# Kernel optimization log

Hardware: AMD Instinct MI355X
Metric: run time of the kernel (lower is better)

## Reference

```python
import jax, jax.numpy as jnp
import numpy as np

# Dims
B, L = 64, 64            # bs*n_vars, patch_num
C, K = 32, 100           # cluster_num, top-k tokens per cluster
D_MODEL, H, D_LLM = 128, 8, 768
D_KEYS = D_MODEL // H    # 16
TEMP = 1.0 / np.sqrt(D_KEYS)
SCALE = 0.02             # param init scale for numerical stability


def setup_inputs() -> dict:
    key = jax.random.key(0)
    ks = jax.random.split(key, 8)
    return {
        "topk_token_embeddings": jax.random.normal(ks[0], (C, K, D_LLM), jnp.float32),
        "ts_emb": jax.random.normal(ks[1], (B, L, D_MODEL), jnp.float32),
        "cluster_probs": jax.random.uniform(ks[2], (B, L, C), jnp.float32),
        # per-cluster projections; last input column is a fused bias (+1 dim)
        "Wq": jax.random.normal(ks[3], (C, H * D_KEYS, D_MODEL + 1), jnp.float32) * SCALE,
        "Wk": jax.random.normal(ks[4], (C, H * D_KEYS, D_LLM + 1), jnp.float32) * SCALE,
        "Wv": jax.random.normal(ks[5], (C, H * D_KEYS, D_LLM + 1), jnp.float32) * SCALE,
        "Wo": jax.random.normal(ks[6], (C, H, D_KEYS, D_LLM), jnp.float32) * SCALE,
        "bo": jax.random.normal(ks[7], (C, D_LLM), jnp.float32) * SCALE,
    }


def reference(topk_token_embeddings, ts_emb, cluster_probs, Wq, Wk, Wv, Wo, bo):
    # Per-cluster Q projection: (B,L,C,H*dk) -> (B,L,C,H,dk)
    q = jnp.einsum('bld,cgd->blcg', ts_emb, Wq[..., :-1]) + Wq[..., -1]
    q = q.reshape(B, L, C, H, D_KEYS)
    # Per-cluster K/V projections: (K,C,H*dk) -> (K,C,H,dk)
    k = jnp.einsum('ckd,cgd->kcg', topk_token_embeddings, Wk[..., :-1]) + Wk[..., -1]
    k = k.reshape(K, C, H, D_KEYS)
    v = jnp.einsum('ckd,cgd->kcg', topk_token_embeddings, Wv[..., :-1]) + Wv[..., -1]
    v = v.reshape(K, C, H, D_KEYS)
    # Attention over token axis k with extra cluster axis c
    att = jnp.einsum('blchd,kchd->bchlk', q, k)          # (B,C,H,L,K)
    att = jax.nn.softmax(TEMP * att, axis=-1)            # dropout is identity in eval
    out = jnp.einsum('bchlk,kchd->bclhd', att, v)        # (B,C,L,H,dk)
    # Per-cluster output projection to d_llm
    aligned = jnp.einsum('bclhd,chde->blce', out, Wo) + bo  # (B,L,C,d_llm)
    # TSAligner: cluster-probability weighted sum over clusters
    fused = jnp.sum(aligned * cluster_probs[:, :, :, None], axis=-2)  # (B,L,d_llm)
    return fused
```

## Files before the change

### kernel.cpp

```cpp
#include <hip/hip_runtime.h>
#include <stdint.h>

#define NB 64
#define NL 64
#define NC 32
#define NK 100
#define NH 8
#define DKEY 16
#define DM 128
#define NG 128
#define DLLM 768
#define KP 4128
#define TEMP 0.25f

typedef __attribute__((ext_vector_type(8))) short bf16x8;
typedef __attribute__((ext_vector_type(4))) short bf16x4;
typedef __attribute__((ext_vector_type(4))) float f32x4;

typedef uint32_t __attribute__((address_space(1))) gu32;
typedef uint32_t __attribute__((address_space(3))) lu32;

__device__ __forceinline__ void gload_lds16(const void* g, void* l) {
    __builtin_amdgcn_global_load_lds((const gu32*)g, (lu32*)l, 16, 0, 0);
}

__device__ __forceinline__ uint16_t f2bf(float f) {
    union { float f; uint32_t i; } x; x.f = f;
    uint32_t r = x.i + 0x7FFFu + ((x.i >> 16) & 1u);
    return (uint16_t)(r >> 16);
}
__device__ __forceinline__ uint32_t pack2(float lo, float hi) {
    return (uint32_t)f2bf(lo) | ((uint32_t)f2bf(hi) << 16);
}
__device__ __forceinline__ uint32_t cvtpk_bf16(float lo, float hi) {
    uint32_t r;
    asm("v_cvt_pk_bf16_f32 %0, %1, %2" : "=v"(r) : "v"(lo), "v"(hi));
    return r;
}

__global__ __launch_bounds__(256) void convert_in_kernel(
    const float* __restrict__ ts,
    const float* __restrict__ Wq,
    uint16_t* __restrict__ tsbf,
    uint16_t* __restrict__ wqbf)
{
    int i = blockIdx.x * 256 + threadIdx.x;
    if (i < 524288) {
        tsbf[i] = f2bf(ts[i]);
    } else {
        int j = i - 524288;
        wqbf[j] = f2bf(Wq[(j >> 7) * 129 + (j & 127)]);
    }
}

__global__ __launch_bounds__(256) void convert_kv_kernel(
    const float* __restrict__ topk,
    const float* __restrict__ Wk,
    const float* __restrict__ Wv,
    uint16_t* __restrict__ topkbf,
    uint16_t* __restrict__ wkbf,
    uint16_t* __restrict__ wvbf)
{
    int r = blockIdx.x;
    int t = threadIdx.x;
    if (r < 3200) {
        if (t < 192) {
            float4 v = *(const float4*)(topk + (size_t)r * 768 + t * 4);
            uint2 u;
            u.x = pack2(v.x, v.y);
            u.y = pack2(v.z, v.w);
            *(uint2*)(topkbf + (size_t)r * 768 + t * 4) = u;
        }
    } else {
        int rr = r - 3200;
        const float* src;
        uint16_t* dst;
        if (rr < 4096) {
            src = Wk + (size_t)rr * 769;
            dst = wkbf + (size_t)rr * 768;
        } else {
            rr -= 4096;
            src = Wv + (size_t)rr * 769;
            dst = wvbf + (size_t)rr * 768;
        }
#pragma unroll
        for (int i = 0; i < 3; ++i)
            dst[t + 256 * i] = f2bf(src[t + 256 * i]);
    }
}

__global__ __launch_bounds__(256) void kv_mfma_kernel(
    const uint16_t* __restrict__ topkbf,
    const uint16_t* __restrict__ wkbf,
    const uint16_t* __restrict__ wvbf,
    const float* __restrict__ Wk,
    const float* __restrict__ Wv,
    uint16_t* __restrict__ kbuf,
    uint16_t* __restrict__ vbufT)
{
    __shared__ short As[2][2048];
    __shared__ short Bs[2][2048];

    int bid = blockIdx.x;
    int nb = bid & 1;
    int mb = (bid >> 1) & 1;
    int c  = (bid >> 2) & 31;
    int which = bid >> 7;

    int tid  = threadIdx.x;
    int lane = tid & 63;
    int w    = tid >> 6;
    int wr   = w >> 1;
    int wc   = w & 1;
    int r16  = lane & 15;
    int kp   = lane >> 4;

    int arow = mb * 64 + w * 16 + r16;
    int brow = nb * 64 + w * 16 + r16;
    const uint16_t* aptr;
    const uint16_t* bptr;
    if (which == 0) {
        aptr = topkbf + ((size_t)(c * 100 + arow)) * 768 + kp * 8;
        bptr = wkbf   + ((size_t)(c * 128 + brow)) * 768 + kp * 8;
    } else {
        aptr = wvbf   + ((size_t)(c * 128 + arow)) * 768 + kp * 8;
        bptr = topkbf + ((size_t)(c * 100 + brow)) * 768 + kp * 8;
    }

    short* adst[2] = { &As[0][w * 512], &As[1][w * 512] };
    short* bdst[2] = { &Bs[0][w * 512], &Bs[1][w * 512] };

    f32x4 acc[2][2] = {};

    gload_lds16(aptr, adst[0]);
    gload_lds16(bptr, bdst[0]);
    __syncthreads();

    int cur = 0;
    for (int kt = 0; kt < 24; ++kt) {
        if (kt < 23) {
            gload_lds16(aptr + (kt + 1) * 32, adst[cur ^ 1]);
            gload_lds16(bptr + (kt + 1) * 32, bdst[cur ^ 1]);
        }
        const short* Ab = As[cur];
        const short* Bb = Bs[cur];
        bf16x8 a0 = *(const bf16x8*)(Ab + (wr * 2 + 0) * 512 + lane * 8);
        bf16x8 a1 = *(const bf16x8*)(Ab + (wr * 2 + 1) * 512 + lane * 8);
        bf16x8 b0 = *(const bf16x8*)(Bb + (wc * 2 + 0) * 512 + lane * 8);
        bf16x8 b1 = *(const bf16x8*)(Bb + (wc * 2 + 1) * 512 + lane * 8);
        acc[0][0] = __builtin_amdgcn_mfma_f32_16x16x32_bf16(a0, b0, acc[0][0], 0, 0, 0);
        acc[0][1] = __builtin_amdgcn_mfma_f32_16x16x32_bf16(a0, b1, acc[0][1], 0, 0, 0);
        acc[1][0] = __builtin_amdgcn_mfma_f32_16x16x32_bf16(a1, b0, acc[1][0], 0, 0, 0);
        acc[1][1] = __builtin_amdgcn_mfma_f32_16x16x32_bf16(a1, b1, acc[1][1], 0, 0, 0);
        __syncthreads();
        cur ^= 1;
    }

    int mbase = mb * 64 + wr * 32 + (lane >> 4) * 4;
    int nbase = nb * 64 + wc * 32 + (lane & 15);

    if (which == 0) {
        float bias0 = Wk[((size_t)c * 128 + nbase)      * 769 + 768];
        float bias1 = Wk[((size_t)c * 128 + nbase + 16) * 769 + 768];
#pragma unroll
        for (int fm = 0; fm < 2; ++fm)
#pragma unroll
            for (int r = 0; r < 4; ++r) {
                int mrow = mbase + fm * 16 + r;
                if (mrow < 112) {
                    kbuf[((size_t)c * 112 + mrow) * 128 + nbase]      = f2bf(acc[fm][0][r] + bias0);
                    kbuf[((size_t)c * 112 + mrow) * 128 + nbase + 16] = f2bf(acc[fm][1][r] + bias1);
                }
            }
    } else {
#pragma unroll
        for (int fm = 0; fm < 2; ++fm)
#pragma unroll
            for (int r = 0; r < 4; ++r) {
                int grow = mbase + fm * 16 + r;
                float bias = Wv[((size_t)c * 128 + grow) * 769 + 768];
#pragma unroll
                for (int fn = 0; fn < 2; ++fn) {
                    int ncol = nbase + fn * 16;
                    uint16_t val = (ncol < NK) ? f2bf(acc[fm][fn][r] + bias) : (uint16_t)0;
                    vbufT[((size_t)c * 128 + grow) * 128 + ncol] = val;
                }
            }
    }
}

__global__ __launch_bounds__(256) void q_proj_mfma_kernel(
    const uint16_t* __restrict__ tsbf,
    const uint16_t* __restrict__ wqbf,
    const float* __restrict__ Wq,
    uint16_t* __restrict__ qbuf)
{
    __shared__ short As[2][2048];
    __shared__ short Bs[2][2048];

    int bid = blockIdx.x;
    int mb = bid & 63;
    int nb = (bid >> 6) & 1;
    int c  = bid >> 7;

    int tid  = threadIdx.x;
    int lane = tid & 63;
    int w    = tid >> 6;
    int wr   = w >> 1;
    int wc   = w & 1;

    int r16 = lane & 15;
    int kp  = lane >> 4;

    const uint16_t* aptr = tsbf + ((size_t)(mb * 64 + w * 16 + r16)) * 128 + kp * 8;
    const uint16_t* bptr = wqbf + ((size_t)(c * 128 + nb * 64 + w * 16 + r16)) * 128 + kp * 8;

    short* adst[2] = { &As[0][w * 512], &As[1][w * 512] };
    short* bdst[2] = { &Bs[0][w * 512], &Bs[1][w * 512] };

    f32x4 acc[2][2] = {};

    gload_lds16(aptr, adst[0]);
    gload_lds16(bptr, bdst[0]);
    __syncthreads();

    int cur = 0;
    for (int kt = 0; kt < 4; ++kt) {
        if (kt < 3) {
            gload_lds16(aptr + (kt + 1) * 32, adst[cur ^ 1]);
            gload_lds16(bptr + (kt + 1) * 32, bdst[cur ^ 1]);
        }
        const short* Ab = As[cur];
        const short* Bb = Bs[cur];
        bf16x8 a0 = *(const bf16x8*)(Ab + (wr * 2 + 0) * 512 + lane * 8);
        bf16x8 a1 = *(const bf16x8*)(Ab + (wr * 2 + 1) * 512 + lane * 8);
        bf16x8 b0 = *(const bf16x8*)(Bb + (wc * 2 + 0) * 512 + lane * 8);
        bf16x8 b1 = *(const bf16x8*)(Bb + (wc * 2 + 1) * 512 + lane * 8);
        acc[0][0] = __builtin_amdgcn_mfma_f32_16x16x32_bf16(a0, b0, acc[0][0], 0, 0, 0);
        acc[0][1] = __builtin_amdgcn_mfma_f32_16x16x32_bf16(a0, b1, acc[0][1], 0, 0, 0);
        acc[1][0] = __builtin_amdgcn_mfma_f32_16x16x32_bf16(a1, b0, acc[1][0], 0, 0, 0);
        acc[1][1] = __builtin_amdgcn_mfma_f32_16x16x32_bf16(a1, b1, acc[1][1], 0, 0, 0);
        __syncthreads();
        cur ^= 1;
    }

    int mbase = mb * 64 + wr * 32 + (lane >> 4) * 4;
    int nbase = nb * 64 + wc * 32 + (lane & 15);
#pragma unroll
    for (int fn = 0; fn < 2; ++fn) {
        int ncol = nbase + fn * 16;
        float bias = Wq[((size_t)c * 128 + ncol) * 129 + 128];
#pragma unroll
        for (int fm = 0; fm < 2; ++fm)
#pragma unroll
            for (int r = 0; r < 4; ++r)
                qbuf[((size_t)c * 4096 + mbase + fm * 16 + r) * 128 + ncol] =
                    f2bf(acc[fm][fn][r] + bias);
    }
}

__global__ __launch_bounds__(256) void attn_mfma_kernel(
    const uint16_t* __restrict__ qbuf,
    const uint16_t* __restrict__ kbuf,
    const uint16_t* __restrict__ vbufT,
    const float* __restrict__ probs,
    uint16_t* __restrict__ wout)
{
    __shared__ short Pl[4][64][128];

    int bid = blockIdx.x;
    int c = bid >> 6;
    int b = bid & 63;
    int tid = threadIdx.x;
    int lane = tid & 63;
    int w = tid >> 6;
    int g = lane >> 4;
    int l15 = lane & 15;
    int swz = l15 << 4;

    float pr_tok = probs[((size_t)b * 64 + lane) * NC + c];

    uint8_t* Pb = (uint8_t*)&Pl[w][0][0];
    bf16x8 zf = {};

    for (int hh = 0; hh < 2; ++hh) {
        int h = w * 2 + hh;

        bf16x8 qb[4];
#pragma unroll
        for (int nt = 0; nt < 4; ++nt) {
            if (g < 2)
                qb[nt] = *(const bf16x8*)&qbuf[((size_t)c * 4096 + b * 64 + nt * 16 + l15) * 128 + h * 16 + g * 8];
            else
                qb[nt] = zf;
        }

        float psum[4] = {0.f, 0.f, 0.f, 0.f};
#pragma unroll
        for (int mt = 0; mt < 7; ++mt) {
            bf16x8 ka;
            if (g < 2)
                ka = *(const bf16x8*)&kbuf[((size_t)c * 112 + mt * 16 + l15) * 128 + h * 16 + g * 8];
            else
                ka = zf;
            f32x4 s[4];
#pragma unroll
            for (int nt = 0; nt < 4; ++nt)
                s[nt] = __builtin_amdgcn_mfma_f32_16x16x32_bf16(ka, qb[nt], (f32x4){0.f,0.f,0.f,0.f}, 0, 0, 0);
            bool valid = (mt < 6) || (g == 0);
#pragma unroll
            for (int nt = 0; nt < 4; ++nt) {
                float p0 = valid ? __expf(s[nt][0] * TEMP) : 0.f;
                float p1 = valid ? __expf(s[nt][1] * TEMP) : 0.f;
                float p2 = valid ? __expf(s[nt][2] * TEMP) : 0.f;
                float p3 = valid ? __expf(s[nt][3] * TEMP) : 0.f;
                psum[nt] += (p0 + p1) + (p2 + p3);
                union { uint32_t u[2]; bf16x4 v; } pk;
                pk.u[0] = cvtpk_bf16(p0, p1);
                pk.u[1] = cvtpk_bf16(p2, p3);
                int l = nt * 16 + l15;
                *(bf16x4*)(Pb + l * 256 + ((mt * 32 + g * 8) ^ swz)) = pk.v;
            }
        }
        {
            bf16x4 z4 = {};
#pragma unroll
            for (int nt = 0; nt < 4; ++nt) {
                int l = nt * 16 + l15;
                *(bf16x4*)(Pb + l * 256 + ((224 + g * 8) ^ swz)) = z4;
            }
        }
        __syncthreads();

        float rsum[4];
#pragma unroll
        for (int nt = 0; nt < 4; ++nt) {
            float t = psum[nt];
            t += __shfl_xor(t, 16);
            t += __shfl_xor(t, 32);
            rsum[nt] = __builtin_amdgcn_rcpf(t);
        }

        f32x4 oacc[4] = {};
#pragma unroll
        for (int ch = 0; ch < 4; ++ch) {
            bf16x8 vb = *(const bf16x8*)&vbufT[((size_t)c * 128 + h * 16 + l15) * 128 + ch * 32 + g * 8];
#pragma unroll
            for (int mt = 0; mt < 4; ++mt) {
                int l = mt * 16 + l15;
                bf16x8 pa = *(const bf16x8*)(Pb + l * 256 + ((ch * 64 + g * 16) ^ swz));
                oacc[mt] = __builtin_amdgcn_mfma_f32_16x16x32_bf16(pa, vb, oacc[mt], 0, 0, 0);
            }
        }
#pragma unroll
        for (int mt = 0; mt < 4; ++mt) {
#pragma unroll
            for (int r = 0; r < 4; ++r) {
                int l = mt * 16 + g * 4 + r;
                float sc = __shfl(pr_tok, l) * __shfl(rsum[mt], g * 4 + r);
                wout[((size_t)b * 64 + l) * KP + c * 128 + h * 16 + l15] =
                    f2bf(oacc[mt][r] * sc);
            }
        }
        __syncthreads();
    }
    if (tid < 64)
        wout[((size_t)b * 64 + tid) * KP + 4096 + c] = f2bf(pr_tok);
}

__global__ __launch_bounds__(256) void convert_wo_kernel(
    const float* __restrict__ Wo,
    const float* __restrict__ bo,
    uint16_t* __restrict__ wobt)
{
    __shared__ float tile[32][65];
    int bid = blockIdx.x;
    int kt = bid / 12;
    int nb = bid % 12;
    int t = threadIdx.x;
    {
        int rr = t >> 3;
        int c0 = (t & 7) * 8;
        int kg = kt * 32 + rr;
        const float* src = (kg < 4096 ? Wo + (size_t)kg * DLLM
                                      : bo + (size_t)(kg - 4096) * DLLM)
                           + nb * 64 + c0;
        float4 v0 = *(const float4*)src;
        float4 v1 = *(const float4*)(src + 4);
        tile[rr][c0 + 0] = v0.x; tile[rr][c0 + 1] = v0.y;
        tile[rr][c0 + 2] = v0.z; tile[rr][c0 + 3] = v0.w;
        tile[rr][c0 + 4] = v1.x; tile[rr][c0 + 5] = v1.y;
        tile[rr][c0 + 6] = v1.z; tile[rr][c0 + 7] = v1.w;
    }
    __syncthreads();
    {
        int n  = t >> 2;
        int k0 = (t & 3) * 8;
        uint4 u;
        u.x = pack2(tile[k0 + 0][n], tile[k0 + 1][n]);
        u.y = pack2(tile[k0 + 2][n], tile[k0 + 3][n]);
        u.z = pack2(tile[k0 + 4][n], tile[k0 + 5][n]);
        u.w = pack2(tile[k0 + 6][n], tile[k0 + 7][n]);
        *(uint4*)&wobt[((size_t)(nb * 64 + n)) * KP + kt * 32 + k0] = u;
    }
}

__global__ __launch_bounds__(256) void fgemm_splitk_kernel(
    const uint16_t* __restrict__ wout,
    const uint16_t* __restrict__ wobt,
    float* __restrict__ part)
{
    __shared__ short As[2][4096];
    __shared__ short Bs[2][4096];

    int bid = blockIdx.x;
    int swz = (bid & 7) * 48 + (bid >> 3);
    int h  = swz / 192;
    int rr = swz - h * 192;
    int mb = rr / 6;
    int nb = rr - mb * 6;

    int tid  = threadIdx.x;
    int lane = tid & 63;
    int w    = tid >> 6;
    int wr   = w >> 1;
    int wc   = w & 1;

    int sg = tid >> 6;
    int skp = (tid >> 4) & 3;
    int sr = tid & 15;
    const uint16_t* aptr = wout + ((size_t)(mb * 128 + sg * 16 + sr)) * KP + h * 2048 + skp * 8;
    const uint16_t* bptr = wobt + ((size_t)(nb * 128 + sg * 16 + sr)) * KP + h * 2048 + skp * 8;

    short* adst[2] = { &As[0][w * 512], &As[1][w * 512] };
    short* bdst[2] = { &Bs[0][w * 512], &Bs[1][w * 512] };

    int nkt = h ? 65 : 64;

    f32x4 acc[4][4] = {};

    gload_lds16(aptr, adst[0]);
    gload_lds16(aptr + (size_t)64 * KP, adst[0] + 2048);
    gload_lds16(bptr, bdst[0]);
    gload_lds16(bptr + (size_t)64 * KP, bdst[0] + 2048);
    __syncthreads();

    int cur = 0;
    for (int kt = 0; kt < nkt; ++kt) {
        if (kt + 1 < nkt) {
            const uint16_t* ap = aptr + (size_t)(kt + 1) * 32;
            const uint16_t* bp = bptr + (size_t)(kt + 1) * 32;
            gload_lds16(ap, adst[cur ^ 1]);
            gload_lds16(ap + (size_t)64 * KP, adst[cur ^ 1] + 2048);
            gload_lds16(bp, bdst[cur ^ 1]);
            gload_lds16(bp + (size_t)64 * KP, bdst[cur ^ 1] + 2048);
        }
        const short* Ab = As[cur];
        const short* Bb = Bs[cur];
        bf16x8 av[4], bv[4];
#pragma unroll
        for (int m = 0; m < 4; ++m)
            av[m] = *(const bf16x8*)(Ab + (wr * 4 + m) * 512 + lane * 8);
#pragma unroll
        for (int n = 0; n < 4; ++n)
            bv[n] = *(const bf16x8*)(Bb + (wc * 4 + n) * 512 + lane * 8);
#pragma unroll
        for (int m = 0; m < 4; ++m)
#pragma unroll
            for (int n = 0; n < 4; ++n)
                acc[m][n] = __builtin_amdgcn_mfma_f32_16x16x32_bf16(av[m], bv[n], acc[m][n], 0, 0, 0);
        __syncthreads();
        cur ^= 1;
    }

    float* P = part + (size_t)h * (4096 * 768);
    int mbase = mb * 128 + wr * 64 + (lane >> 4) * 4;
    int nbase = nb * 128 + wc * 64 + (lane & 15);
#pragma unroll
    for (int m = 0; m < 4; ++m)
#pragma unroll
        for (int n = 0; n < 4; ++n)
#pragma unroll
            for (int r = 0; r < 4; ++r)
                P[(size_t)(mbase + m * 16 + r) * DLLM + nbase + n * 16] =
                    acc[m][n][r];
}

__global__ __launch_bounds__(256) void reduce_out_kernel(
    const float* __restrict__ part,
    float* __restrict__ out)
{
    int i = (blockIdx.x * 256 + threadIdx.x) * 4;
    float4 a = *(const float4*)(part + i);
    float4 b = *(const float4*)(part + 4096 * 768 + i);
    float4 s;
    s.x = a.x + b.x; s.y = a.y + b.y; s.z = a.z + b.z; s.w = a.w + b.w;
    *(float4*)(out + i) = s;
}

extern "C" void kernel_launch(void* const* d_in, const int* in_sizes, int n_in,
                              void* d_out, int out_size, void* d_ws, size_t ws_size,
                              hipStream_t stream) {
    const float* topk  = (const float*)d_in[0];
    const float* ts    = (const float*)d_in[1];
    const float* probs = (const float*)d_in[2];
    const float* Wq    = (const float*)d_in[3];
    const float* Wk    = (const float*)d_in[4];
    const float* Wv    = (const float*)d_in[5];
    const float* Wo    = (const float*)d_in[6];
    const float* bo    = (const float*)d_in[7];
    float* out = (float*)d_out;

    uint16_t* ws    = (uint16_t*)d_ws;
    uint16_t* kbuf  = ws;
    uint16_t* vbufT = ws + 458752;
    uint16_t* qbuf  = ws + 983040;
    uint16_t* wout  = ws + 983040 + 16777216;
    uint16_t* tsbf   = wout;
    uint16_t* wqbf   = wout + 524288;
    uint16_t* topkbf = wout + 1048576;
    uint16_t* wkbf   = wout + 1048576 + 2457600;
    uint16_t* wvbf   = wout + 1048576 + 2457600 + 3145728;
    uint16_t* wobt = qbuf;
    float*    part = (float*)(qbuf + 3170304);

    convert_in_kernel<<<4096, 256, 0, stream>>>(ts, Wq, tsbf, wqbf);
    convert_kv_kernel<<<11392, 256, 0, stream>>>(topk, Wk, Wv, topkbf, wkbf, wvbf);
    kv_mfma_kernel<<<256, 256, 0, stream>>>(topkbf, wkbf, wvbf, Wk, Wv, kbuf, vbufT);
    q_proj_mfma_kernel<<<4096, 256, 0, stream>>>(tsbf, wqbf, Wq, qbuf);
    attn_mfma_kernel<<<2048, 256, 0, stream>>>(qbuf, kbuf, vbufT, probs, wout);
    convert_wo_kernel<<<1548, 256, 0, stream>>>(Wo, bo, wobt);
    fgemm_splitk_kernel<<<384, 256, 0, stream>>>(wout, wobt, part);
    reduce_out_kernel<<<3072, 256, 0, stream>>>(part, out);
}
```

Measured before the change: 169.9 us.

## Enlarge Q-projection tiles, fold softmax scale into Q, compute row sums via MFMA

The Q projection kernel now computes a 128x128 output tile per block with a 4x4 MFMA fragment grid per wave, cutting the grid to a quarter of its size and improving operand reuse. The softmax temperature and log2(e) are folded into the stored Q values, so the attention kernel can use exp2 directly. Softmax denominators are now computed by an extra MFMA against a ones vector instead of cross-lane shuffles, which lets the workgroup barriers be replaced by per-wave LDS waitcnts since each wave only uses its own P buffer. This trades extra MFMA work and higher register pressure for fewer barriers and less ALU work.

Result: no change. 172.4 us (+1.5%).

```diff
diff --git a/kernel.cpp b/kernel.cpp
--- a/kernel.cpp
+++ b/kernel.cpp
@@ -12,6 +12,7 @@
 #define DLLM 768
 #define KP 4128
 #define TEMP 0.25f
+#define QSCL 0.3606737602222409f
 
 typedef __attribute__((ext_vector_type(8))) short bf16x8;
 typedef __attribute__((ext_vector_type(4))) short bf16x4;
@@ -195,13 +196,12 @@
     const float* __restrict__ Wq,
     uint16_t* __restrict__ qbuf)
 {
-    __shared__ short As[2][2048];
-    __shared__ short Bs[2][2048];
+    __shared__ short As[2][4096];
+    __shared__ short Bs[2][4096];
 
     int bid = blockIdx.x;
-    int mb = bid & 63;
-    int nb = (bid >> 6) & 1;
-    int c  = bid >> 7;
+    int mb = bid & 31;
+    int c  = bid >> 5;
 
     int tid  = threadIdx.x;
     int lane = tid & 63;
@@ -209,53 +209,63 @@
     int wr   = w >> 1;
     int wc   = w & 1;
 
-    int r16 = lane & 15;
-    int kp  = lane >> 4;
-
-    const uint16_t* aptr = tsbf + ((size_t)(mb * 64 + w * 16 + r16)) * 128 + kp * 8;
-    const uint16_t* bptr = wqbf + ((size_t)(c * 128 + nb * 64 + w * 16 + r16)) * 128 + kp * 8;
+    int sg  = tid >> 6;
+    int skp = (tid >> 4) & 3;
+    int sr  = tid & 15;
+    const uint16_t* aptr = tsbf + ((size_t)(mb * 128 + sg * 16 + sr)) * 128 + skp * 8;
+    const uint16_t* bptr = wqbf + ((size_t)(c * 128 + sg * 16 + sr)) * 128 + skp * 8;
 
     short* adst[2] = { &As[0][w * 512], &As[1][w * 512] };
     short* bdst[2] = { &Bs[0][w * 512], &Bs[1][w * 512] };
 
-    f32x4 acc[2][2] = {};
+    f32x4 acc[4][4] = {};
 
     gload_lds16(aptr, adst[0]);
+    gload_lds16(aptr + (size_t)64 * 128, adst[0] + 2048);
     gload_lds16(bptr, bdst[0]);
+    gload_lds16(bptr + (size_t)64 * 128, bdst[0] + 2048);
     __syncthreads();
 
     int cur = 0;
     for (int kt = 0; kt < 4; ++kt) {
         if (kt < 3) {
-            gload_lds16(aptr + (kt + 1) * 32, adst[cur ^ 1]);
-            gload_lds16(bptr + (kt + 1) * 32, bdst[cur ^ 1]);
+            const uint16_t* ap = aptr + (kt + 1) * 32;
+            const uint16_t* bp = bptr + (kt + 1) * 32;
+            gload_lds16(ap, adst[cur ^ 1]);
+            gload_lds16(ap + (size_t)64 * 128, adst[cur ^ 1] + 2048);
+            gload_lds16(bp, bdst[cur ^ 1]);
+            gload_lds16(bp + (size_t)64 * 128, bdst[cur ^ 1] + 2048);
         }
         const short* Ab = As[cur];
         const short* Bb = Bs[cur];
-        bf16x8 a0 = *(const bf16x8*)(Ab + (wr * 2 + 0) * 512 + lane * 8);
-        bf16x8 a1 = *(const bf16x8*)(Ab + (wr * 2 + 1) * 512 + lane * 8);
-        bf16x8 b0 = *(const bf16x8*)(Bb + (wc * 2 + 0) * 512 + lane * 8);
-        bf16x8 b1 = *(const bf16x8*)(Bb + (wc * 2 + 1) * 512 + lane * 8);
-        acc[0][0] = __builtin_amdgcn_mfma_f32_16x16x32_bf16(a0, b0, acc[0][0], 0, 0, 0);
-        acc[0][1] = __builtin_amdgcn_mfma_f32_16x16x32_bf16(a0, b1, acc[0][1], 0, 0, 0);
-        acc[1][0] = __builtin_amdgcn_mfma_f32_16x16x32_bf16(a1, b0, acc[1][0], 0, 0, 0);
-        acc[1][1] = __builtin_amdgcn_mfma_f32_16x16x32_bf16(a1, b1, acc[1][1], 0, 0, 0);
+        bf16x8 av[4], bv[4];
+#pragma unroll
+        for (int m = 0; m < 4; ++m)
+            av[m] = *(const bf16x8*)(Ab + (wr * 4 + m) * 512 + lane * 8);
+#pragma unroll
+        for (int n = 0; n < 4; ++n)
+            bv[n] = *(const bf16x8*)(Bb + (wc * 4 + n) * 512 + lane * 8);
+#pragma unroll
+        for (int m = 0; m < 4; ++m)
+#pragma unroll
+            for (int n = 0; n < 4; ++n)
+                acc[m][n] = __builtin_amdgcn_mfma_f32_16x16x32_bf16(av[m], bv[n], acc[m][n], 0, 0, 0);
         __syncthreads();
         cur ^= 1;
     }
 
-    int mbase = mb * 64 + wr * 32 + (lane >> 4) * 4;
-    int nbase = nb * 64 + wc * 32 + (lane & 15);
-#pragma unroll
-    for (int fn = 0; fn < 2; ++fn) {
-        int ncol = nbase + fn * 16;
+    int mbase = mb * 128 + wr * 64 + (lane >> 4) * 4;
+    int nfix  = wc * 64 + (lane & 15);
+#pragma unroll
+    for (int n = 0; n < 4; ++n) {
+        int ncol = nfix + n * 16;
         float bias = Wq[((size_t)c * 128 + ncol) * 129 + 128];
 #pragma unroll
-        for (int fm = 0; fm < 2; ++fm)
+        for (int m = 0; m < 4; ++m)
 #pragma unroll
             for (int r = 0; r < 4; ++r)
-                qbuf[((size_t)c * 4096 + mbase + fm * 16 + r) * 128 + ncol] =
-                    f2bf(acc[fm][fn][r] + bias);
+                qbuf[((size_t)c * 4096 + mbase + m * 16 + r) * 128 + ncol] =
+                    f2bf((acc[m][n][r] + bias) * QSCL);
     }
 }
 
@@ -282,6 +292,8 @@
 
     uint8_t* Pb = (uint8_t*)&Pl[w][0][0];
     bf16x8 zf = {};
+    const short ob = (short)0x3F80;
+    bf16x8 ones = { ob, ob, ob, ob, ob, ob, ob, ob };
 
     for (int hh = 0; hh < 2; ++hh) {
         int h = w * 2 + hh;
@@ -295,7 +307,6 @@
                 qb[nt] = zf;
         }
 
-        float psum[4] = {0.f, 0.f, 0.f, 0.f};
 #pragma unroll
         for (int mt = 0; mt < 7; ++mt) {
             bf16x8 ka;
@@ -310,11 +321,10 @@
             bool valid = (mt < 6) || (g == 0);
 #pragma unroll
             for (int nt = 0; nt < 4; ++nt) {
-                float p0 = valid ? __expf(s[nt][0] * TEMP) : 0.f;
-                float p1 = valid ? __expf(s[nt][1] * TEMP) : 0.f;
-                float p2 = valid ? __expf(s[nt][2] * TEMP) : 0.f;
-                float p3 = valid ? __expf(s[nt][3] * TEMP) : 0.f;
-                psum[nt] += (p0 + p1) + (p2 + p3);
+                float p0 = valid ? __builtin_exp2f(s[nt][0]) : 0.f;
+                float p1 = valid ? __builtin_exp2f(s[nt][1]) : 0.f;
+                float p2 = valid ? __builtin_exp2f(s[nt][2]) : 0.f;
+                float p3 = valid ? __builtin_exp2f(s[nt][3]) : 0.f;
                 union { uint32_t u[2]; bf16x4 v; } pk;
                 pk.u[0] = cvtpk_bf16(p0, p1);
                 pk.u[1] = cvtpk_bf16(p2, p3);
@@ -330,18 +340,10 @@
                 *(bf16x4*)(Pb + l * 256 + ((224 + g * 8) ^ swz)) = z4;
             }
         }
-        __syncthreads();
-
-        float rsum[4];
-#pragma unroll
-        for (int nt = 0; nt < 4; ++nt) {
-            float t = psum[nt];
-            t += __shfl_xor(t, 16);
-            t += __shfl_xor(t, 32);
-            rsum[nt] = __builtin_amdgcn_rcpf(t);
-        }
+        asm volatile("s_waitcnt lgkmcnt(0)" ::: "memory");
 
         f32x4 oacc[4] = {};
+        f32x4 osum[4] = {};
 #pragma unroll
         for (int ch = 0; ch < 4; ++ch) {
             bf16x8 vb = *(const bf16x8*)&vbufT[((size_t)c * 128 + h * 16 + l15) * 128 + ch * 32 + g * 8];
@@ -350,6 +352,7 @@
                 int l = mt * 16 + l15;
                 bf16x8 pa = *(const bf16x8*)(Pb + l * 256 + ((ch * 64 + g * 16) ^ swz));
                 oacc[mt] = __builtin_amdgcn_mfma_f32_16x16x32_bf16(pa, vb, oacc[mt], 0, 0, 0);
+                osum[mt] = __builtin_amdgcn_mfma_f32_16x16x32_bf16(pa, ones, osum[mt], 0, 0, 0);
             }
         }
 #pragma unroll
@@ -357,12 +360,12 @@
 #pragma unroll
             for (int r = 0; r < 4; ++r) {
                 int l = mt * 16 + g * 4 + r;
-                float sc = __shfl(pr_tok, l) * __shfl(rsum[mt], g * 4 + r);
+                float sc = __shfl(pr_tok, l) * __builtin_amdgcn_rcpf(osum[mt][r]);
                 wout[((size_t)b * 64 + l) * KP + c * 128 + h * 16 + l15] =
                     f2bf(oacc[mt][r] * sc);
             }
         }
-        __syncthreads();
+        asm volatile("s_waitcnt lgkmcnt(0)" ::: "memory");
     }
     if (tid < 64)
         wout[((size_t)b * 64 + tid) * KP + 4096 + c] = f2bf(pr_tok);
@@ -527,7 +530,7 @@
     convert_in_kernel<<<4096, 256, 0, stream>>>(ts, Wq, tsbf, wqbf);
     convert_kv_kernel<<<11392, 256, 0, stream>>>(topk, Wk, Wv, topkbf, wkbf, wvbf);
     kv_mfma_kernel<<<256, 256, 0, stream>>>(topkbf, wkbf, wvbf, Wk, Wv, kbuf, vbufT);
-    q_proj_mfma_kernel<<<4096, 256, 0, stream>>>(tsbf, wqbf, Wq, qbuf);
+    q_proj_mfma_kernel<<<1024, 256, 0, stream>>>(tsbf, wqbf, Wq, qbuf);
     attn_mfma_kernel<<<2048, 256, 0, stream>>>(qbuf, kbuf, vbufT, probs, wout);
     convert_wo_kernel<<<1548, 256, 0, stream>>>(Wo, bo, wobt);
     fgemm_splitk_kernel<<<384, 256, 0, stream>>>(wout, wobt, part);
```
